# Optimization experiments

Measured on AMD Instinct MI355X. Metric: run time of the kernel, lower is better.

Reference implementation:

```python
import jax, jax.numpy as jnp
import numpy as np

H = 32          # query heads
KV = 8          # key/value heads
HD = 128        # head_dim
EPS = 1e-6
SCALE = HD ** -0.5


def _rms_norm(x, w):
    # per-head RMSNorm over last dim in fp32
    xf = x.astype(jnp.float32)
    var = jnp.mean(xf * xf, axis=-1, keepdims=True)
    return (w * (xf * jax.lax.rsqrt(var + EPS))).astype(x.dtype)


def _rotate_half(x):
    x1, x2 = jnp.split(x, 2, axis=-1)
    return jnp.concatenate([-x2, x1], axis=-1)


def setup_inputs() -> dict:
    key = jax.random.key(0)
    ks = jax.random.split(key, 8)
    B, S, D = 1, 2048, 4096
    hidden_states = jax.random.normal(ks[0], (B, S, D), dtype=jnp.float32)
    # rotary tables (half head dim), realistic frequencies
    pos = jnp.arange(S, dtype=jnp.float32)
    inv_freq = 1.0 / (1e6 ** (jnp.arange(0, HD, 2, dtype=jnp.float32) / HD))
    ang = pos[:, None] * inv_freq[None, :]          # [S, HD/2]
    cos = jnp.broadcast_to(jnp.cos(ang)[None], (B, S, HD // 2))
    sin = jnp.broadcast_to(jnp.sin(ang)[None], (B, S, HD // 2))
    # additive causal mask [B,1,S,S]
    causal = jnp.tril(jnp.ones((S, S), dtype=bool))
    attention_mask = jnp.where(causal, 0.0, -1e9).astype(jnp.float32)[None, None]
    attention_mask = jnp.broadcast_to(attention_mask, (B, 1, S, S))
    std = 0.02
    Wq = jax.random.normal(ks[1], (H * HD, D), dtype=jnp.float32) * std
    Wk = jax.random.normal(ks[2], (KV * HD, D), dtype=jnp.float32) * std
    Wv = jax.random.normal(ks[3], (KV * HD, D), dtype=jnp.float32) * std
    Wo = jax.random.normal(ks[4], (D, H * HD), dtype=jnp.float32) * std
    q_norm_w = jnp.ones((HD,), dtype=jnp.float32)
    k_norm_w = jnp.ones((HD,), dtype=jnp.float32)
    return {"hidden_states": hidden_states, "cos": cos, "sin": sin,
            "attention_mask": attention_mask, "Wq": Wq, "Wk": Wk, "Wv": Wv,
            "Wo": Wo, "q_norm_w": q_norm_w, "k_norm_w": k_norm_w}


def reference(hidden_states, cos, sin, attention_mask, Wq, Wk, Wv, Wo, q_norm_w, k_norm_w):
    B, S, D = hidden_states.shape
    # QKV projections (no bias), reshape to heads, per-head RMSNorm on q/k
    q = (hidden_states @ Wq.T).reshape(B, S, H, HD)
    k = (hidden_states @ Wk.T).reshape(B, S, KV, HD)
    v = (hidden_states @ Wv.T).reshape(B, S, KV, HD)
    q = _rms_norm(q, q_norm_w).transpose(0, 2, 1, 3)   # [B,H,S,HD]
    k = _rms_norm(k, k_norm_w).transpose(0, 2, 1, 3)   # [B,KV,S,HD]
    v = v.transpose(0, 2, 1, 3)                        # [B,KV,S,HD]
    # RoPE: cos/sin [B,S,HD/2] -> [B,1,S,HD]
    cos2 = jnp.concatenate([cos, cos], axis=-1)[:, None]
    sin2 = jnp.concatenate([sin, sin], axis=-1)[:, None]
    q = q * cos2 + _rotate_half(q) * sin2
    k = k * cos2 + _rotate_half(k) * sin2
    # GQA repeat kv
    n_rep = H // KV
    k = jnp.repeat(k, n_rep, axis=1)                   # [B,H,S,HD]
    v = jnp.repeat(v, n_rep, axis=1)
    # eager attention, fp32 softmax
    scores = jnp.einsum('bhqd,bhkd->bhqk', q, k) * SCALE + attention_mask
    probs = jax.nn.softmax(scores.astype(jnp.float32), axis=-1).astype(q.dtype)
    attn = jnp.einsum('bhqk,bhkd->bhqd', probs, v)
    attn = attn.transpose(0, 2, 1, 3).reshape(B, S, H * HD)
    return attn @ Wo.T
```

## Files before the change

### kernel.cpp

```cpp
#include <hip/hip_runtime.h>
#include <hip/hip_bf16.h>


#define S_LEN 2048
#define D_MODEL 4096
#define NH 32
#define NKV 8
#define HD 128
#define EPS 1e-6f
#define SCALE 0.08838834764831845f
#define NEG_BIG (-1e30f)

typedef __bf16 bf16_t;
typedef __bf16 bf16x8 __attribute__((ext_vector_type(8)));
typedef __bf16 bf16x4 __attribute__((ext_vector_type(4)));
typedef float f32x4 __attribute__((ext_vector_type(4)));

__device__ __forceinline__ bool input_is_bf16(const void* qw) {
    return ((*(const unsigned*)qw) & 0xFFFFu) == 0x3F80u;
}

__device__ __forceinline__ void gload_lds16(const void* g, void* l) {
    __builtin_amdgcn_global_load_lds(
        (const __attribute__((address_space(1))) void*)g,
        (__attribute__((address_space(3))) void*)l, 16, 0, 0);
}

template<bool BF16>
__device__ __forceinline__ float ld1(const void* p, size_t i) {
    if constexpr (BF16) return (float)((const bf16_t*)p)[i];
    else return ((const float*)p)[i];
}
template<bool BF16>
__device__ __forceinline__ void st1(void* p, size_t i, float v) {
    if constexpr (BF16) ((bf16_t*)p)[i] = (bf16_t)v;
    else ((float*)p)[i] = v;
}

__device__ __forceinline__ bf16x8 cvt8(const float* src) {
    float4 a = *(const float4*)src, b = *(const float4*)(src + 4);
    bf16x8 r;
    r[0] = (bf16_t)a.x; r[1] = (bf16_t)a.y; r[2] = (bf16_t)a.z; r[3] = (bf16_t)a.w;
    r[4] = (bf16_t)b.x; r[5] = (bf16_t)b.y; r[6] = (bf16_t)b.z; r[7] = (bf16_t)b.w;
    return r;
}

__global__ __launch_bounds__(256) void conv_kernel(const void* src, const void* qw,
                                                   bf16_t* __restrict__ dst) {
    size_t i = ((size_t)blockIdx.x * 256 + threadIdx.x) * 8;
    if (input_is_bf16(qw)) {
        *(bf16x8*)&dst[i] = *(const bf16x8*)((const bf16_t*)src + i);
    } else {
        *(bf16x8*)&dst[i] = cvt8((const float*)src + i);
    }
}

__global__ __launch_bounds__(256) void convw_kernel(
    const void* Wq, const void* Wk, const void* Wv, const void* Wo,
    const void* qw, bf16_t* __restrict__ dq, bf16_t* __restrict__ dk,
    bf16_t* __restrict__ dv, bf16_t* __restrict__ dwo) {
    int b = blockIdx.x;
    const void* src; bf16_t* dst; size_t base;
    if (b < 8192)       { src = Wq; dst = dq;  base = (size_t)b * 2048; }
    else if (b < 10240) { src = Wk; dst = dk;  base = (size_t)(b - 8192) * 2048; }
    else if (b < 12288) { src = Wv; dst = dv;  base = (size_t)(b - 10240) * 2048; }
    else                { src = Wo; dst = dwo; base = (size_t)(b - 12288) * 2048; }
    size_t i = base + (size_t)threadIdx.x * 8;
    if (input_is_bf16(qw)) {
        *(bf16x8*)&dst[i] = *(const bf16x8*)((const bf16_t*)src + i);
    } else {
        *(bf16x8*)&dst[i] = cvt8((const float*)src + i);
    }
}

__device__ __forceinline__ void stage_a(const bf16_t* __restrict__ src, int m0,
                                        int k0, bf16_t* lds_a, int lane, int w) {
    #pragma unroll
    for (int i = 0; i < 2; ++i) {
        int r16 = w * 2 + i;
        gload_lds16(src + (size_t)(m0 + r16 * 16 + (lane >> 2)) * D_MODEL + k0 + (lane & 3) * 8,
                    &lds_a[r16 * 512]);
    }
}

template<bool WB>
__device__ __forceinline__ void stage_w(const void* W, size_t nrow0, int k0,
                                        bf16_t* lds_b, int tid, int lane, int w) {
    if constexpr (WB) {
        const bf16_t* Wb = (const bf16_t*)W + nrow0 * D_MODEL;
        #pragma unroll
        for (int i = 0; i < 2; ++i) {
            int r16 = w * 2 + i;
            gload_lds16(Wb + (size_t)(r16 * 16 + (lane >> 2)) * D_MODEL + k0 + (lane & 3) * 8,
                        &lds_b[r16 * 512]);
        }
    } else {
        const float* Wf = (const float*)W + nrow0 * D_MODEL;
        #pragma unroll
        for (int j = 0; j < 2; ++j) {
            int e = j * 2048 + tid * 8;
            int row = e >> 5, kk = e & 31;
            *(bf16x8*)&lds_b[e] = cvt8(Wf + (size_t)row * D_MODEL + k0 + kk);
        }
    }
}

template<bool BF16, bool WB>
__device__ void qkv_body(
    const bf16_t* __restrict__ hsb, const void* cosp, const void* sinp,
    const void* Wq, const void* Wk, const void* Wv,
    const void* qw, const void* kw,
    bf16_t* __restrict__ qn, bf16_t* __restrict__ kn, bf16_t* __restrict__ vt,
    bf16_t* lds_a, bf16_t* lds_b)
{
    const int tid = threadIdx.x;
    const int lane = tid & 63;
    const int w = tid >> 6;
    const int c = lane & 15;
    const int g = lane >> 4;
    const int m0 = blockIdx.x * 128;
    const int slot = blockIdx.y;

    const void* Wbase; int type, h;
    if (slot < 32)      { type = 0; h = slot;      Wbase = Wq; }
    else if (slot < 40) { type = 1; h = slot - 32; Wbase = Wk; }
    else                { type = 2; h = slot - 40; Wbase = Wv; }
    const size_t nrow0 = (size_t)h * HD;

    f32x4 acc[2][8] = {};

    stage_a(hsb, m0, 0, lds_a, lane, w);
    stage_w<WB>(Wbase, nrow0, 0, lds_b, tid, lane, w);
    __syncthreads();

    int cur = 0;
    for (int k0 = 0; k0 < D_MODEL; k0 += 32) {
        int nxt = cur ^ 1;
        if (k0 + 32 < D_MODEL) {
            stage_a(hsb, m0, k0 + 32, lds_a + nxt * 4096, lane, w);
            stage_w<WB>(Wbase, nrow0, k0 + 32, lds_b + nxt * 4096, tid, lane, w);
        }
        const bf16_t* la = lds_a + cur * 4096;
        const bf16_t* lb = lds_b + cur * 4096;
        bf16x8 af0 = *(const bf16x8*)&la[(w * 32 + c) * 32 + g * 8];
        bf16x8 af1 = *(const bf16x8*)&la[(w * 32 + 16 + c) * 32 + g * 8];
        #pragma unroll
        for (int ni = 0; ni < 8; ++ni) {
            bf16x8 bfr = *(const bf16x8*)&lb[(ni * 16 + c) * 32 + g * 8];
            acc[0][ni] = __builtin_amdgcn_mfma_f32_16x16x32_bf16(af0, bfr, acc[0][ni], 0, 0, 0);
            acc[1][ni] = __builtin_amdgcn_mfma_f32_16x16x32_bf16(af1, bfr, acc[1][ni], 0, 0, 0);
        }
        __syncthreads();
        cur = nxt;
    }

    if (type == 2) {
        #pragma unroll
        for (int mi = 0; mi < 2; ++mi) {
            int s = m0 + w * 32 + mi * 16 + g * 4;
            #pragma unroll
            for (int ni = 0; ni < 8; ++ni) {
                bf16x4 pk;
                #pragma unroll
                for (int r = 0; r < 4; ++r) pk[r] = (bf16_t)acc[mi][ni][r];
                *(bf16x4*)&vt[((size_t)h * HD + ni * 16 + c) * S_LEN + s] = pk;
            }
        }
        return;
    }

    const void* nw = (type == 0) ? qw : kw;
    bf16_t* outb = (type == 0) ? (qn + (size_t)h * S_LEN * HD)
                               : (kn + (size_t)h * S_LEN * HD);
    #pragma unroll
    for (int mi = 0; mi < 2; ++mi) {
        float ss[4];
        #pragma unroll
        for (int r = 0; r < 4; ++r) {
            float p = 0.f;
            #pragma unroll
            for (int ni = 0; ni < 8; ++ni) p += acc[mi][ni][r] * acc[mi][ni][r];
            p += __shfl_xor(p, 1); p += __shfl_xor(p, 2);
            p += __shfl_xor(p, 4); p += __shfl_xor(p, 8);
            ss[r] = rsqrtf(p * (1.f / HD) + EPS);
        }
        float v[8][4];
        #pragma unroll
        for (int ni = 0; ni < 8; ++ni) {
            float wg = ld1<BF16>(nw, ni * 16 + c);
            #pragma unroll
            for (int r = 0; r < 4; ++r) v[ni][r] = acc[mi][ni][r] * ss[r] * wg;
        }
        #pragma unroll
        for (int r = 0; r < 4; ++r) {
            int s = m0 + w * 32 + mi * 16 + g * 4 + r;
            #pragma unroll
            for (int t = 0; t < 4; ++t) {
                int nn = t * 16 + c;
                float co = ld1<BF16>(cosp, (size_t)s * 64 + nn);
                float si = ld1<BF16>(sinp, (size_t)s * 64 + nn);
                float x1 = v[t][r], x2 = v[t + 4][r];
                v[t][r]     = x1 * co - x2 * si;
                v[t + 4][r] = x2 * co + x1 * si;
            }
        }
        #pragma unroll
        for (int t = 0; t < 8; ++t)
            #pragma unroll
            for (int r = 0; r < 4; ++r) {
                int s = m0 + w * 32 + mi * 16 + g * 4 + r;
                outb[(size_t)s * HD + t * 16 + c] = (bf16_t)v[t][r];
            }
    }
}

__global__ __launch_bounds__(256) void qkv_kernel(
    const bf16_t* __restrict__ hsb, const void* cosp, const void* sinp,
    const void* Wq, const void* Wk, const void* Wv,
    const void* qw, const void* kw,
    bf16_t* __restrict__ qn, bf16_t* __restrict__ kn, bf16_t* __restrict__ vt,
    int wconv)
{
    __shared__ bf16_t lds_a[2][128 * 32];
    __shared__ bf16_t lds_b[2][128 * 32];
    bool ib = input_is_bf16(qw);
    if (wconv) {
        if (ib) qkv_body<true,  true>(hsb, cosp, sinp, Wq, Wk, Wv, qw, kw, qn, kn, vt, &lds_a[0][0], &lds_b[0][0]);
        else    qkv_body<false, true>(hsb, cosp, sinp, Wq, Wk, Wv, qw, kw, qn, kn, vt, &lds_a[0][0], &lds_b[0][0]);
    } else {
        if (ib) qkv_body<true,  true>(hsb, cosp, sinp, Wq, Wk, Wv, qw, kw, qn, kn, vt, &lds_a[0][0], &lds_b[0][0]);
        else    qkv_body<false, false>(hsb, cosp, sinp, Wq, Wk, Wv, qw, kw, qn, kn, vt, &lds_a[0][0], &lds_b[0][0]);
    }
}

__global__ __launch_bounds__(256) void attn_kernel(
    const bf16_t* __restrict__ qn, const bf16_t* __restrict__ kn,
    const bf16_t* __restrict__ vt, bf16_t* __restrict__ attnb)
{
    __shared__ bf16_t lds_k[32 * 128];
    __shared__ bf16_t lds_v[128 * 32];

    const int lane = threadIdx.x & 63;
    const int w = threadIdx.x >> 6;
    const int c = lane & 15;
    const int g = lane >> 4;
    const int h = blockIdx.y;
    const int hk = h >> 2;
    const int xa = blockIdx.x;
    const int lr = lane >> 2;
    const int lk = (lane & 3) * 8;

    const int qrow0 = xa * 64 + w * 16;
    const int qrow1 = (31 - xa) * 64 + w * 16;
    const int kmaxA = xa * 64 + 64;
    const int kmaxB = (31 - xa) * 64 + 64;

    const bf16_t* kb_base = kn + (size_t)hk * S_LEN * HD;
    const bf16_t* vt_base = vt + (size_t)hk * HD * S_LEN;

    bf16x8 qf[2][4];
    #pragma unroll
    for (int ks = 0; ks < 4; ++ks) {
        qf[0][ks] = *(const bf16x8*)(qn + ((size_t)h * S_LEN + qrow0 + c) * HD + ks * 32 + g * 8);
        qf[1][ks] = *(const bf16x8*)(qn + ((size_t)h * S_LEN + qrow1 + c) * HD + ks * 32 + g * 8);
    }

    f32x4 o[2][8] = {};
    float m_cur[2] = {NEG_BIG, NEG_BIG};
    float l_cur[2] = {0.f, 0.f};

    for (int kb = 0; kb < kmaxB; kb += 32) {
        const bool liveA = (kb < kmaxA);
        __syncthreads();
        #pragma unroll
        for (int i = 0; i < 2; ++i) {
            int t16 = w * 2 + i;
            gload_lds16(kb_base + (size_t)(kb + t16 * 4 + g) * HD + c * 8,
                        &lds_k[t16 * 512]);
            gload_lds16(vt_base + (size_t)(t16 * 16 + lr) * S_LEN + kb + lk,
                        &lds_v[t16 * 512]);
        }
        __syncthreads();

        float p[2][2][4];
        #pragma unroll
        for (int u = 0; u < 2; ++u) {
            f32x4 sacc0 = {}, sacc1 = {};
            #pragma unroll
            for (int ks = 0; ks < 4; ++ks) {
                bf16x8 kf = *(const bf16x8*)&lds_k[(u * 16 + c) * 128 + ks * 32 + g * 8];
                if (liveA)
                    sacc0 = __builtin_amdgcn_mfma_f32_16x16x32_bf16(kf, qf[0][ks], sacc0, 0, 0, 0);
                sacc1 = __builtin_amdgcn_mfma_f32_16x16x32_bf16(kf, qf[1][ks], sacc1, 0, 0, 0);
            }
            #pragma unroll
            for (int r = 0; r < 4; ++r) {
                int key_abs = kb + u * 16 + g * 4 + r;
                p[0][u][r] = (key_abs <= qrow0 + c) ? sacc0[r] * SCALE : NEG_BIG;
                p[1][u][r] = (key_abs <= qrow1 + c) ? sacc1[r] * SCALE : NEG_BIG;
            }
        }

        bf16x8 pb[2];
        #pragma unroll
        for (int qt = 0; qt < 2; ++qt) {
            if (qt == 0 && !liveA) continue;
            float mx = NEG_BIG;
            #pragma unroll
            for (int u = 0; u < 2; ++u)
                #pragma unroll
                for (int r = 0; r < 4; ++r) mx = fmaxf(mx, p[qt][u][r]);
            mx = fmaxf(mx, __shfl_xor(mx, 16));
            mx = fmaxf(mx, __shfl_xor(mx, 32));
            float m_new = fmaxf(m_cur[qt], mx);
            float alpha = __expf(m_cur[qt] - m_new);
            float lsum = 0.f;
            #pragma unroll
            for (int u = 0; u < 2; ++u)
                #pragma unroll
                for (int r = 0; r < 4; ++r) {
                    float e = __expf(p[qt][u][r] - m_new);
                    p[qt][u][r] = e;
                    lsum += e;
                }
            lsum += __shfl_xor(lsum, 16);
            lsum += __shfl_xor(lsum, 32);
            l_cur[qt] = l_cur[qt] * alpha + lsum;
            m_cur[qt] = m_new;
            #pragma unroll
            for (int dt = 0; dt < 8; ++dt) o[qt][dt] *= alpha;
            #pragma unroll
            for (int j = 0; j < 8; ++j) {
                int src = (((g * 2 + (j >> 2)) & 3) << 4) | c;
                float v0 = __shfl(p[qt][0][j & 3], src);
                float v1 = __shfl(p[qt][1][j & 3], src);
                pb[qt][j] = (bf16_t)((g >= 2) ? v1 : v0);
            }
        }
        #pragma unroll
        for (int dt = 0; dt < 8; ++dt) {
            bf16x8 vf = *(const bf16x8*)&lds_v[(dt * 16 + c) * 32 + g * 8];
            if (liveA)
                o[0][dt] = __builtin_amdgcn_mfma_f32_16x16x32_bf16(vf, pb[0], o[0][dt], 0, 0, 0);
            o[1][dt] = __builtin_amdgcn_mfma_f32_16x16x32_bf16(vf, pb[1], o[1][dt], 0, 0, 0);
        }
    }

    #pragma unroll
    for (int qt = 0; qt < 2; ++qt) {
        float inv_l = 1.f / l_cur[qt];
        int q = (qt == 0 ? qrow0 : qrow1) + c;
        #pragma unroll
        for (int dt = 0; dt < 8; ++dt) {
            bf16x4 pk;
            #pragma unroll
            for (int r = 0; r < 4; ++r) pk[r] = (bf16_t)(o[qt][dt][r] * inv_l);
            *(bf16x4*)&attnb[(size_t)q * D_MODEL + h * HD + dt * 16 + g * 4] = pk;
        }
    }
}

template<bool BF16, bool WB>
__device__ void out_body(const bf16_t* __restrict__ attnb, const void* Wo,
                         void* outp, bf16_t* lds_a, bf16_t* lds_b)
{
    const int tid = threadIdx.x;
    const int lane = tid & 63;
    const int w = tid >> 6;
    const int c = lane & 15;
    const int g = lane >> 4;
    const int wm = w >> 1, wn = w & 1;
    const int m0 = blockIdx.x * 128, n0 = blockIdx.y * 128;

    f32x4 acc[4][4] = {};

    stage_a(attnb, m0, 0, lds_a, lane, w);
    stage_w<WB>(Wo, (size_t)n0, 0, lds_b, tid, lane, w);
    __syncthreads();

    int cur = 0;
    for (int k0 = 0; k0 < D_MODEL; k0 += 32) {
        int nxt = cur ^ 1;
        if (k0 + 32 < D_MODEL) {
            stage_a(attnb, m0, k0 + 32, lds_a + nxt * 4096, lane, w);
            stage_w<WB>(Wo, (size_t)n0, k0 + 32, lds_b + nxt * 4096, tid, lane, w);
        }
        const bf16_t* la = lds_a + cur * 4096;
        const bf16_t* lb = lds_b + cur * 4096;
        bf16x8 af[4], bfr[4];
        #pragma unroll
        for (int i = 0; i < 4; ++i) {
            af[i]  = *(const bf16x8*)&la[(wm * 64 + i * 16 + c) * 32 + g * 8];
            bfr[i] = *(const bf16x8*)&lb[(wn * 64 + i * 16 + c) * 32 + g * 8];
        }
        #pragma unroll
        for (int mi = 0; mi < 4; ++mi)
            #pragma unroll
            for (int ni = 0; ni < 4; ++ni)
                acc[mi][ni] = __builtin_amdgcn_mfma_f32_16x16x32_bf16(af[mi], bfr[ni], acc[mi][ni], 0, 0, 0);
        __syncthreads();
        cur = nxt;
    }
    #pragma unroll
    for (int mi = 0; mi < 4; ++mi)
        #pragma unroll
        for (int ni = 0; ni < 4; ++ni)
            #pragma unroll
            for (int r = 0; r < 4; ++r)
                st1<BF16>(outp, (size_t)(m0 + wm * 64 + mi * 16 + g * 4 + r) * D_MODEL
                                 + n0 + wn * 64 + ni * 16 + c, acc[mi][ni][r]);
}

__global__ __launch_bounds__(256) void out_kernel(
    const bf16_t* __restrict__ attnb, const void* Wo, const void* qw, void* outp,
    int wconv)
{
    __shared__ bf16_t lds_a[2][128 * 32];
    __shared__ bf16_t lds_b[2][128 * 32];
    bool ib = input_is_bf16(qw);
    if (wconv) {
        if (ib) out_body<true,  true>(attnb, Wo, outp, &lds_a[0][0], &lds_b[0][0]);
        else    out_body<false, true>(attnb, Wo, outp, &lds_a[0][0], &lds_b[0][0]);
    } else {
        if (ib) out_body<true,  true>(attnb, Wo, outp, &lds_a[0][0], &lds_b[0][0]);
        else    out_body<false, false>(attnb, Wo, outp, &lds_a[0][0], &lds_b[0][0]);
    }
}

extern "C" void kernel_launch(void* const* d_in, const int* in_sizes, int n_in,
                              void* d_out, int out_size, void* d_ws, size_t ws_size,
                              hipStream_t stream) {
    const void* hs   = d_in[0];
    const void* cosp = d_in[1];
    const void* sinp = d_in[2];
    const void* Wq = d_in[4];
    const void* Wk = d_in[5];
    const void* Wv = d_in[6];
    const void* Wo = d_in[7];
    const void* qw = d_in[8];
    const void* kw = d_in[9];

    const size_t NEED   = 41943040ull;
    const size_t NEED_W = NEED + 83886080ull;
    if (ws_size < NEED) return;
    const int wconv = (ws_size >= NEED_W) ? 1 : 0;

    char* ws = (char*)d_ws;
    bf16_t* buf0 = (bf16_t*)(ws);
    bf16_t* qn   = (bf16_t*)(ws + 16777216);
    bf16_t* kn   = (bf16_t*)(ws + 2 * 16777216);
    bf16_t* vt   = (bf16_t*)(ws + 2 * 16777216 + 4194304);

    conv_kernel<<<dim3(4096), 256, 0, stream>>>(hs, qw, buf0);

    if (wconv) {
        bf16_t* dq  = (bf16_t*)(ws + NEED);
        bf16_t* dk  = (bf16_t*)(ws + NEED + 33554432ull);
        bf16_t* dv  = (bf16_t*)(ws + NEED + 33554432ull + 8388608ull);
        bf16_t* dwo = (bf16_t*)(ws + NEED + 33554432ull + 2*8388608ull);
        convw_kernel<<<dim3(20480), 256, 0, stream>>>(Wq, Wk, Wv, Wo, qw, dq, dk, dv, dwo);
        qkv_kernel<<<dim3(16, 48), 256, 0, stream>>>(buf0, cosp, sinp, dq, dk, dv, qw, kw,
                                                     qn, kn, vt, 1);
        attn_kernel<<<dim3(16, 32), 256, 0, stream>>>(qn, kn, vt, buf0);
        out_kernel<<<dim3(16, 32), 256, 0, stream>>>(buf0, dwo, qw, d_out, 1);
    } else {
        qkv_kernel<<<dim3(16, 48), 256, 0, stream>>>(buf0, cosp, sinp, Wq, Wk, Wv, qw, kw,
                                                     qn, kn, vt, 0);
        attn_kernel<<<dim3(16, 32), 256, 0, stream>>>(qn, kn, vt, buf0);
        out_kernel<<<dim3(16, 32), 256, 0, stream>>>(buf0, Wo, qw, d_out, 0);
    }
}
```

Measured before the change: 727.3 us.

## Triple-buffer GEMM LDS staging with vmcnt-based waits in QKV and output kernels

After: 743.0 us. 1.02x slower.

```diff
diff --git a/kernel.cpp b/kernel.cpp
--- a/kernel.cpp
+++ b/kernel.cpp
@@ -24,6 +24,13 @@
     __builtin_amdgcn_global_load_lds(
         (const __attribute__((address_space(1))) void*)g,
         (__attribute__((address_space(3))) void*)l, 16, 0, 0);
+}
+
+__device__ __forceinline__ void vm_wait4() {
+    asm volatile("s_waitcnt vmcnt(4)" ::: "memory");
+}
+__device__ __forceinline__ void vm_wait0() {
+    asm volatile("s_waitcnt vmcnt(0)" ::: "memory");
 }
 
 template<bool BF16>
@@ -129,29 +136,58 @@
 
     f32x4 acc[2][8] = {};
 
-    stage_a(hsb, m0, 0, lds_a, lane, w);
-    stage_w<WB>(Wbase, nrow0, 0, lds_b, tid, lane, w);
-    __syncthreads();
-
-    int cur = 0;
-    for (int k0 = 0; k0 < D_MODEL; k0 += 32) {
-        int nxt = cur ^ 1;
-        if (k0 + 32 < D_MODEL) {
-            stage_a(hsb, m0, k0 + 32, lds_a + nxt * 4096, lane, w);
-            stage_w<WB>(Wbase, nrow0, k0 + 32, lds_b + nxt * 4096, tid, lane, w);
-        }
-        const bf16_t* la = lds_a + cur * 4096;
-        const bf16_t* lb = lds_b + cur * 4096;
-        bf16x8 af0 = *(const bf16x8*)&la[(w * 32 + c) * 32 + g * 8];
-        bf16x8 af1 = *(const bf16x8*)&la[(w * 32 + 16 + c) * 32 + g * 8];
-        #pragma unroll
-        for (int ni = 0; ni < 8; ++ni) {
-            bf16x8 bfr = *(const bf16x8*)&lb[(ni * 16 + c) * 32 + g * 8];
-            acc[0][ni] = __builtin_amdgcn_mfma_f32_16x16x32_bf16(af0, bfr, acc[0][ni], 0, 0, 0);
-            acc[1][ni] = __builtin_amdgcn_mfma_f32_16x16x32_bf16(af1, bfr, acc[1][ni], 0, 0, 0);
-        }
+    if constexpr (WB) {
+        stage_a(hsb, m0, 0, lds_a, lane, w);
+        stage_w<true>(Wbase, nrow0, 0, lds_b, tid, lane, w);
+        stage_a(hsb, m0, 32, lds_a + 4096, lane, w);
+        stage_w<true>(Wbase, nrow0, 32, lds_b + 4096, tid, lane, w);
+        vm_wait4();
+        __builtin_amdgcn_s_barrier();
+
+        for (int it = 0; it < 128; ++it) {
+            const int pf = it + 2;
+            if (pf < 128) {
+                const int pb = pf % 3;
+                stage_a(hsb, m0, pf * 32, lds_a + pb * 4096, lane, w);
+                stage_w<true>(Wbase, nrow0, pf * 32, lds_b + pb * 4096, tid, lane, w);
+            }
+            const bf16_t* la = lds_a + (it % 3) * 4096;
+            const bf16_t* lb = lds_b + (it % 3) * 4096;
+            bf16x8 af0 = *(const bf16x8*)&la[(w * 32 + c) * 32 + g * 8];
+            bf16x8 af1 = *(const bf16x8*)&la[(w * 32 + 16 + c) * 32 + g * 8];
+            #pragma unroll
+            for (int ni = 0; ni < 8; ++ni) {
+                bf16x8 bfr = *(const bf16x8*)&lb[(ni * 16 + c) * 32 + g * 8];
+                acc[0][ni] = __builtin_amdgcn_mfma_f32_16x16x32_bf16(af0, bfr, acc[0][ni], 0, 0, 0);
+                acc[1][ni] = __builtin_amdgcn_mfma_f32_16x16x32_bf16(af1, bfr, acc[1][ni], 0, 0, 0);
+            }
+            if (pf < 128) vm_wait4(); else vm_wait0();
+            __builtin_amdgcn_s_barrier();
+        }
+    } else {
+        stage_a(hsb, m0, 0, lds_a, lane, w);
+        stage_w<false>(Wbase, nrow0, 0, lds_b, tid, lane, w);
         __syncthreads();
-        cur = nxt;
+        int cur = 0;
+        for (int k0 = 0; k0 < D_MODEL; k0 += 32) {
+            int nxt = cur ^ 1;
+            if (k0 + 32 < D_MODEL) {
+                stage_a(hsb, m0, k0 + 32, lds_a + nxt * 4096, lane, w);
+                stage_w<false>(Wbase, nrow0, k0 + 32, lds_b + nxt * 4096, tid, lane, w);
+            }
+            const bf16_t* la = lds_a + cur * 4096;
+            const bf16_t* lb = lds_b + cur * 4096;
+            bf16x8 af0 = *(const bf16x8*)&la[(w * 32 + c) * 32 + g * 8];
+            bf16x8 af1 = *(const bf16x8*)&la[(w * 32 + 16 + c) * 32 + g * 8];
+            #pragma unroll
+            for (int ni = 0; ni < 8; ++ni) {
+                bf16x8 bfr = *(const bf16x8*)&lb[(ni * 16 + c) * 32 + g * 8];
+                acc[0][ni] = __builtin_amdgcn_mfma_f32_16x16x32_bf16(af0, bfr, acc[0][ni], 0, 0, 0);
+                acc[1][ni] = __builtin_amdgcn_mfma_f32_16x16x32_bf16(af1, bfr, acc[1][ni], 0, 0, 0);
+            }
+            __syncthreads();
+            cur = nxt;
+        }
     }
 
     if (type == 2) {
@@ -221,8 +257,8 @@
     bf16_t* __restrict__ qn, bf16_t* __restrict__ kn, bf16_t* __restrict__ vt,
     int wconv)
 {
-    __shared__ bf16_t lds_a[2][128 * 32];
-    __shared__ bf16_t lds_b[2][128 * 32];
+    __shared__ bf16_t lds_a[3][128 * 32];
+    __shared__ bf16_t lds_b[3][128 * 32];
     bool ib = input_is_bf16(qw);
     if (wconv) {
         if (ib) qkv_body<true,  true>(hsb, cosp, sinp, Wq, Wk, Wv, qw, kw, qn, kn, vt, &lds_a[0][0], &lds_b[0][0]);
@@ -374,32 +410,64 @@
 
     f32x4 acc[4][4] = {};
 
-    stage_a(attnb, m0, 0, lds_a, lane, w);
-    stage_w<WB>(Wo, (size_t)n0, 0, lds_b, tid, lane, w);
-    __syncthreads();
-
-    int cur = 0;
-    for (int k0 = 0; k0 < D_MODEL; k0 += 32) {
-        int nxt = cur ^ 1;
-        if (k0 + 32 < D_MODEL) {
-            stage_a(attnb, m0, k0 + 32, lds_a + nxt * 4096, lane, w);
-            stage_w<WB>(Wo, (size_t)n0, k0 + 32, lds_b + nxt * 4096, tid, lane, w);
-        }
-        const bf16_t* la = lds_a + cur * 4096;
-        const bf16_t* lb = lds_b + cur * 4096;
-        bf16x8 af[4], bfr[4];
-        #pragma unroll
-        for (int i = 0; i < 4; ++i) {
-            af[i]  = *(const bf16x8*)&la[(wm * 64 + i * 16 + c) * 32 + g * 8];
-            bfr[i] = *(const bf16x8*)&lb[(wn * 64 + i * 16 + c) * 32 + g * 8];
-        }
-        #pragma unroll
-        for (int mi = 0; mi < 4; ++mi)
-            #pragma unroll
-            for (int ni = 0; ni < 4; ++ni)
-                acc[mi][ni] = __builtin_amdgcn_mfma_f32_16x16x32_bf16(af[mi], bfr[ni], acc[mi][ni], 0, 0, 0);
+    if constexpr (WB) {
+        stage_a(attnb, m0, 0, lds_a, lane, w);
+        stage_w<true>(Wo, (size_t)n0, 0, lds_b, tid, lane, w);
+        stage_a(attnb, m0, 32, lds_a + 4096, lane, w);
+        stage_w<true>(Wo, (size_t)n0, 32, lds_b + 4096, tid, lane, w);
+        vm_wait4();
+        __builtin_amdgcn_s_barrier();
+
+        for (int it = 0; it < 128; ++it) {
+            const int pf = it + 2;
+            if (pf < 128) {
+                const int pb = pf % 3;
+                stage_a(attnb, m0, pf * 32, lds_a + pb * 4096, lane, w);
+                stage_w<true>(Wo, (size_t)n0, pf * 32, lds_b + pb * 4096, tid, lane, w);
+            }
+            const bf16_t* la = lds_a + (it % 3) * 4096;
+            const bf16_t* lb = lds_b + (it % 3) * 4096;
+            bf16x8 af[4], bfr[4];
+            #pragma unroll
+            for (int i = 0; i < 4; ++i) {
+                af[i]  = *(const bf16x8*)&la[(wm * 64 + i * 16 + c) * 32 + g * 8];
+                bfr[i] = *(const bf16x8*)&lb[(wn * 64 + i * 16 + c) * 32 + g * 8];
+            }
+            #pragma unroll
+            for (int mi = 0; mi < 4; ++mi)
+                #pragma unroll
+                for (int ni = 0; ni < 4; ++ni)
+                    acc[mi][ni] = __builtin_amdgcn_mfma_f32_16x16x32_bf16(af[mi], bfr[ni], acc[mi][ni], 0, 0, 0);
+            if (pf < 128) vm_wait4(); else vm_wait0();
+            __builtin_amdgcn_s_barrier();
+        }
+    } else {
+        stage_a(attnb, m0, 0, lds_a, lane, w);
+        stage_w<false>(Wo, (size_t)n0, 0, lds_b, tid, lane, w);
         __syncthreads();
-        cur = nxt;
+        int cur = 0;
+        for (int k0 = 0; k0 < D_MODEL; k0 += 32) {
+            int nxt = cur ^ 1;
+            if (k0 + 32 < D_MODEL) {
+                stage_a(attnb, m0, k0 + 32, lds_a + nxt * 4096, lane, w);
+                stage_w<false>(Wo, (size_t)n0, k0 + 32, lds_b + nxt * 4096, tid, lane, w);
+            }
+            const bf16_t* la = lds_a + cur * 4096;
+            const bf16_t* lb = lds_b + cur * 4096;
+            bf16x8 af[4], bfr[4];
+            #pragma unroll
+            for (int i = 0; i < 4; ++i) {
+                af[i]  = *(const bf16x8*)&la[(wm * 64 + i * 16 + c) * 32 + g * 8];
+                bfr[i] = *(const bf16x8*)&lb[(wn * 64 + i * 16 + c) * 32 + g * 8];
+            }
+            #pragma unroll
+            for (int mi = 0; mi < 4; ++mi)
+                #pragma unroll
+                for (int ni = 0; ni < 4; ++ni)
+                    acc[mi][ni] = __builtin_amdgcn_mfma_f32_16x16x32_bf16(af[mi], bfr[ni], acc[mi][ni], 0, 0, 0);
+            __syncthreads();
+            cur = nxt;
+        }
     }
     #pragma unroll
     for (int mi = 0; mi < 4; ++mi)
@@ -415,8 +483,8 @@
     const bf16_t* __restrict__ attnb, const void* Wo, const void* qw, void* outp,
     int wconv)
 {
-    __shared__ bf16_t lds_a[2][128 * 32];
-    __shared__ bf16_t lds_b[2][128 * 32];
+    __shared__ bf16_t lds_a[3][128 * 32];
+    __shared__ bf16_t lds_b[3][128 * 32];
     bool ib = input_is_bf16(qw);
     if (wconv) {
         if (ib) out_body<true,  true>(attnb, Wo, outp, &lds_a[0][0], &lds_b[0][0]);
```
